# Kernel optimization log

Hardware: AMD Instinct MI355X
Metric: run time of the kernel (lower is better)

## Reference

```python
import jax, jax.numpy as jnp
import numpy as np

EPS = 1e-5  # InstanceNorm2d default eps


def setup_inputs() -> dict:
    key = jax.random.key(0)
    ks = jax.random.split(key, 5)
    B, T, C, N, H = 4, 8, 256, 196, 4
    s = 1.0 / np.sqrt(C)
    return {
        "emb": jax.random.normal(ks[0], (B, T, C, N), dtype=jnp.float32),
        "Wq": jax.random.normal(ks[1], (H, C, C), dtype=jnp.float32) * s,
        "Wk": jax.random.normal(ks[2], (H, C, C), dtype=jnp.float32) * s,
        "Wv": jax.random.normal(ks[3], (H, C, C), dtype=jnp.float32) * s,
        "Wo": jax.random.normal(ks[4], (C, C), dtype=jnp.float32) * s,
    }


def reference(emb, Wq, Wk, Wv, Wo):
    B, T, C, N = emb.shape
    S = T * N  # KV_size
    # emb.permute(0,1,3,2).view(B, T*N, C)
    x = jnp.transpose(emb, (0, 1, 3, 2)).reshape(B, S, C)
    # per-head full-width Linear projections (nn.Linear: y = x @ W.T)
    Q = jnp.einsum("bsc,hdc->bhsd", x, Wq)  # [B,H,S,C]
    K = jnp.einsum("bsc,hdc->bhsd", x, Wk)
    V = jnp.einsum("bsc,hdc->bhsd", x, Wv)
    scores = jnp.einsum("bhsd,bhtd->bhst", Q, K) / jnp.sqrt(jnp.float32(S))
    # InstanceNorm2d over each [S,S] map per (batch, head), no affine, biased var
    mean = jnp.mean(scores, axis=(-2, -1), keepdims=True)
    var = jnp.var(scores, axis=(-2, -1), keepdims=True)
    normed = (scores - mean) * jax.lax.rsqrt(var + EPS)
    probs = jax.nn.softmax(normed, axis=-1)  # attn_dropout: eval-mode identity
    ctx = jnp.einsum("bhst,bhtd->bhsd", probs, V)  # [B,H,S,C]
    ctx = jnp.mean(ctx, axis=1)  # mean over heads -> [B,S,C]
    O1 = jnp.einsum("bsc,dc->bsd", ctx, Wo)  # out Linear; proj_dropout identity
    # .view(-1, num_frames, num_channels, num_patches) on contiguous [B, T*N, C]
    return O1.reshape(B, T, C, N)
```

## Files before the change

kernel.cpp:

```cpp
#include <hip/hip_runtime.h>
#include <stdint.h>

typedef unsigned short u16;

#define Bb 4
#define Hh 4
#define Tt 8
#define Cc 256
#define NP 196
#define Ss 1568
#define SCALE_S 0.0252538136f

typedef __attribute__((ext_vector_type(4))) float floatx4;
typedef __attribute__((ext_vector_type(8))) short shortx8;

__device__ __forceinline__ float bf2f(u16 u) {
    union { unsigned u; float f; } v; v.u = ((unsigned)u) << 16; return v.f;
}
__device__ __forceinline__ u16 f2bf(float f) {
    union { float f; unsigned u; } v; v.f = f;
    unsigned r = v.u + 0x7FFFu + ((v.u >> 16) & 1u);
    return (u16)(r >> 16);
}

__global__ __launch_bounds__(256) void k_convw(const float* __restrict__ src, u16* __restrict__ dst, int n) {
    int i = blockIdx.x * 256 + threadIdx.x;
    if (i < n) dst[i] = f2bf(src[i]);
}

__device__ __forceinline__ void mfma_step(const u16* As, const u16* Bs, int lane,
                                          int wm, int wn, floatx4 acc[4][4]) {
    const int r15 = lane & 15;
    const int kq  = (lane >> 4) << 3;
    shortx8 a[4], b[4];
#pragma unroll
    for (int i = 0; i < 4; ++i)
        a[i] = *(const shortx8*)(As + (wm * 64 + i * 16 + r15) * 32 + kq);
#pragma unroll
    for (int j = 0; j < 4; ++j)
        b[j] = *(const shortx8*)(Bs + (wn * 64 + j * 16 + r15) * 32 + kq);
#pragma unroll
    for (int i = 0; i < 4; ++i)
#pragma unroll
        for (int j = 0; j < 4; ++j)
            acc[i][j] = __builtin_amdgcn_mfma_f32_16x16x32_bf16(a[i], b[j], acc[i][j], 0, 0, 0);
}

__device__ __forceinline__ void gemm_bt_core(const u16* A, const u16* Bm, int lda, int ldb,
                                             int mbase, int mlast, int nbase, int nlast,
                                             int KD, u16* As, u16* Bs, floatx4 acc[4][4]) {
    int tid = threadIdx.x;
    int lane = tid & 63, wave = tid >> 6, wm = wave >> 1, wn = wave & 1;
    int row0 = tid >> 2, row1 = 64 + (tid >> 2);
    int cole = (tid & 3) << 3;
    for (int k0 = 0; k0 < KD; k0 += 32) {
        int ga0 = mbase + row0; ga0 = ga0 <= mlast ? ga0 : mlast;
        int ga1 = mbase + row1; ga1 = ga1 <= mlast ? ga1 : mlast;
        int gb0 = nbase + row0; gb0 = gb0 <= nlast ? gb0 : nlast;
        int gb1 = nbase + row1; gb1 = gb1 <= nlast ? gb1 : nlast;
        shortx8 va0 = *(const shortx8*)(A  + (size_t)ga0 * lda + k0 + cole);
        shortx8 va1 = *(const shortx8*)(A  + (size_t)ga1 * lda + k0 + cole);
        shortx8 vb0 = *(const shortx8*)(Bm + (size_t)gb0 * ldb + k0 + cole);
        shortx8 vb1 = *(const shortx8*)(Bm + (size_t)gb1 * ldb + k0 + cole);
        __syncthreads();
        *(shortx8*)(As + row0 * 32 + cole) = va0;
        *(shortx8*)(As + row1 * 32 + cole) = va1;
        *(shortx8*)(Bs + row0 * 32 + cole) = vb0;
        *(shortx8*)(Bs + row1 * 32 + cole) = vb1;
        __syncthreads();
        mfma_step(As, Bs, lane, wm, wn, acc);
    }
}

__global__ void k_transpose(const float* __restrict__ emb, u16* __restrict__ x) {
    __shared__ u16 tile[32][33];
    int bt = blockIdx.z;
    int c0 = blockIdx.y * 32, n0 = blockIdx.x * 32;
    const float* src = emb + (size_t)bt * Cc * NP;
#pragma unroll
    for (int rr = 0; rr < 32; rr += 8) {
        int c = c0 + threadIdx.y + rr;
        int n = n0 + threadIdx.x;
        u16 v = 0;
        if (n < NP) v = f2bf(src[(size_t)c * NP + n]);
        tile[threadIdx.y + rr][threadIdx.x] = v;
    }
    __syncthreads();
    int b = bt / Tt, t = bt % Tt;
    u16* dst = x + ((size_t)b * Ss + (size_t)t * NP) * Cc;
#pragma unroll
    for (int rr = 0; rr < 32; rr += 8) {
        int n = n0 + threadIdx.y + rr;
        int c = c0 + threadIdx.x;
        if (n < NP) dst[(size_t)n * Cc + c] = tile[threadIdx.x][threadIdx.y + rr];
    }
}

__global__ __launch_bounds__(256) void k_qkv(const u16* __restrict__ x,
                                             const u16* __restrict__ Wq,
                                             const u16* __restrict__ Wk,
                                             const u16* __restrict__ Wv,
                                             u16* __restrict__ Q, u16* __restrict__ Kb,
                                             u16* __restrict__ Vt) {
    __shared__ __align__(16) u16 As[128 * 32], Bs[128 * 32];
    floatx4 acc[4][4];
#pragma unroll
    for (int i = 0; i < 4; ++i)
#pragma unroll
        for (int j = 0; j < 4; ++j) acc[i][j] = (floatx4)(0.f);
    int z = blockIdx.z;
    int qkv = z >> 4, bh = z & 15, b = bh >> 2, h = bh & 3;
    const u16* A = x + (size_t)b * Ss * Cc;
    const u16* W = (qkv == 0 ? Wq : (qkv == 1 ? Wk : Wv)) + (size_t)h * Cc * Cc;
    int mbase = blockIdx.y * 128, nbase = blockIdx.x * 128;
    gemm_bt_core(A, W, Cc, Cc, mbase, Ss - 1, nbase, Cc - 1, Cc, As, Bs, acc);

    int tid = threadIdx.x, lane = tid & 63, wave = tid >> 6, wm = wave >> 1, wn = wave & 1;
    int rq = (lane >> 4) << 2, cn = lane & 15;
    if (qkv < 2) {
        u16* out = (qkv == 0 ? Q : Kb) + (size_t)bh * Ss * Cc;
#pragma unroll
        for (int i = 0; i < 4; ++i) {
            int mb = mbase + wm * 64 + i * 16 + rq;
#pragma unroll
            for (int j = 0; j < 4; ++j) {
                int n = nbase + wn * 64 + j * 16 + cn;
#pragma unroll
                for (int r = 0; r < 4; ++r) {
                    int m = mb + r;
                    if (m < Ss) out[(size_t)m * Cc + n] = f2bf(acc[i][j][r]);
                }
            }
        }
    } else {
        u16* out = Vt + (size_t)bh * Cc * Ss;
#pragma unroll
        for (int i = 0; i < 4; ++i) {
            int m0 = mbase + wm * 64 + i * 16 + rq;
            if (m0 < Ss) {
#pragma unroll
                for (int j = 0; j < 4; ++j) {
                    int n = nbase + wn * 64 + j * 16 + cn;
                    ushort4 v;
                    v.x = f2bf(acc[i][j][0]); v.y = f2bf(acc[i][j][1]);
                    v.z = f2bf(acc[i][j][2]); v.w = f2bf(acc[i][j][3]);
                    *(ushort4*)(out + (size_t)n * Ss + m0) = v;
                }
            }
        }
    }
}

__global__ __launch_bounds__(256) void k_scores(const u16* __restrict__ Q,
                                                const u16* __restrict__ Kb,
                                                u16* __restrict__ Sc, float* __restrict__ stats) {
    __shared__ __align__(16) u16 As[128 * 32], Bs[128 * 32];
    __shared__ float sred[8];
    floatx4 acc[4][4];
#pragma unroll
    for (int i = 0; i < 4; ++i)
#pragma unroll
        for (int j = 0; j < 4; ++j) acc[i][j] = (floatx4)(0.f);
    int bh = blockIdx.z;
    const u16* A  = Q  + (size_t)bh * Ss * Cc;
    const u16* Bm = Kb + (size_t)bh * Ss * Cc;
    int mbase = blockIdx.y * 128, nbase = blockIdx.x * 128;
    gemm_bt_core(A, Bm, Cc, Cc, mbase, Ss - 1, nbase, Ss - 1, Cc, As, Bs, acc);

    int tid = threadIdx.x, lane = tid & 63, wave = tid >> 6, wm = wave >> 1, wn = wave & 1;
    int rq = (lane >> 4) << 2, cn = lane & 15;
    u16* out = Sc + (size_t)bh * Ss * Ss;
    float lsum = 0.f, lsq = 0.f;
#pragma unroll
    for (int i = 0; i < 4; ++i) {
        int mb = mbase + wm * 64 + i * 16 + rq;
#pragma unroll
        for (int j = 0; j < 4; ++j) {
            int n = nbase + wn * 64 + j * 16 + cn;
            bool nv = n < Ss;
#pragma unroll
            for (int r = 0; r < 4; ++r) {
                int m = mb + r;
                if (nv && m < Ss) {
                    float v = acc[i][j][r] * SCALE_S;
                    out[(size_t)m * Ss + n] = f2bf(v);
                    lsum += v; lsq += v * v;
                }
            }
        }
    }
#pragma unroll
    for (int mk = 1; mk <= 32; mk <<= 1) { lsum += __shfl_xor(lsum, mk); lsq += __shfl_xor(lsq, mk); }
    if (lane == 0) { sred[wave] = lsum; sred[4 + wave] = lsq; }
    __syncthreads();
    if (tid == 0) atomicAdd(&stats[bh * 4 + 0], sred[0] + sred[1] + sred[2] + sred[3]);
    if (tid == 1) atomicAdd(&stats[bh * 4 + 1], sred[4] + sred[5] + sred[6] + sred[7]);
}

__global__ void k_stats(float* __restrict__ stats) {
    int i = threadIdx.x;
    if (i < 16) {
        float inv  = 1.f / ((float)Ss * (float)Ss);
        float mean = stats[i * 4] * inv;
        float var  = stats[i * 4 + 1] * inv - mean * mean;
        var = fmaxf(var, 0.f);
        stats[i * 4 + 2] = mean;
        stats[i * 4 + 3] = rsqrtf(var + 1e-5f);
    }
}

__global__ __launch_bounds__(256) void k_pv(const u16* __restrict__ Sc,
                                            const u16* __restrict__ Vt,
                                            const float* __restrict__ stats,
                                            u16* __restrict__ ctx) {
    __shared__ __align__(16) u16 As[128 * 32], Bs[128 * 32];
    __shared__ float rs[128];
    floatx4 acc[4][4];
#pragma unroll
    for (int i = 0; i < 4; ++i)
#pragma unroll
        for (int j = 0; j < 4; ++j) acc[i][j] = (floatx4)(0.f);
    int bh = blockIdx.z;
    float mean = stats[bh * 4 + 2], istd = stats[bh * 4 + 3];
    float aa = istd * 1.44269504f;
    float bb = -mean * aa;
    const u16* A  = Sc + (size_t)bh * Ss * Ss;
    const u16* Bm = Vt + (size_t)bh * Cc * Ss;
    int mbase = blockIdx.y * 128, nbase = blockIdx.x * 128;
    int tid = threadIdx.x, lane = tid & 63, wave = tid >> 6, wm = wave >> 1, wn = wave & 1;
    int row0 = tid >> 2, row1 = 64 + (tid >> 2);
    int cole = (tid & 3) << 3;
    float rsum0 = 0.f, rsum1 = 0.f;

    for (int k0 = 0; k0 < Ss; k0 += 32) {
        int ga0 = mbase + row0; ga0 = ga0 <= Ss - 1 ? ga0 : Ss - 1;
        int ga1 = mbase + row1; ga1 = ga1 <= Ss - 1 ? ga1 : Ss - 1;
        shortx8 v0 = *(const shortx8*)(A + (size_t)ga0 * Ss + k0 + cole);
        shortx8 v1 = *(const shortx8*)(A + (size_t)ga1 * Ss + k0 + cole);
        shortx8 vb0 = *(const shortx8*)(Bm + (size_t)(nbase + row0) * Ss + k0 + cole);
        shortx8 vb1 = *(const shortx8*)(Bm + (size_t)(nbase + row1) * Ss + k0 + cole);
        shortx8 o0, o1;
        float p0 = 0.f, p1 = 0.f;
#pragma unroll
        for (int e = 0; e < 8; ++e) {
            float f0 = bf2f((u16)v0[e]);
            float e0 = exp2f(f0 * aa + bb);
            p0 += e0; o0[e] = (short)f2bf(e0);
            float f1 = bf2f((u16)v1[e]);
            float e1 = exp2f(f1 * aa + bb);
            p1 += e1; o1[e] = (short)f2bf(e1);
        }
        rsum0 += p0; rsum1 += p1;
        __syncthreads();
        *(shortx8*)(As + row0 * 32 + cole) = o0;
        *(shortx8*)(As + row1 * 32 + cole) = o1;
        *(shortx8*)(Bs + row0 * 32 + cole) = vb0;
        *(shortx8*)(Bs + row1 * 32 + cole) = vb1;
        __syncthreads();
        mfma_step(As, Bs, lane, wm, wn, acc);
    }
    rsum0 += __shfl_xor(rsum0, 1); rsum0 += __shfl_xor(rsum0, 2);
    rsum1 += __shfl_xor(rsum1, 1); rsum1 += __shfl_xor(rsum1, 2);
    __syncthreads();
    if ((tid & 3) == 0) { rs[tid >> 2] = rsum0; rs[64 + (tid >> 2)] = rsum1; }
    __syncthreads();

    u16* out = ctx + (size_t)bh * Ss * Cc;
    int rq = (lane >> 4) << 2, cn = lane & 15;
#pragma unroll
    for (int i = 0; i < 4; ++i) {
        int ml = wm * 64 + i * 16 + rq;
#pragma unroll
        for (int r = 0; r < 4; ++r) {
            int m = mbase + ml + r;
            if (m < Ss) {
                float invs = 1.f / rs[ml + r];
#pragma unroll
                for (int j = 0; j < 4; ++j) {
                    int n = nbase + wn * 64 + j * 16 + cn;
                    out[(size_t)m * Cc + n] = f2bf(acc[i][j][r] * invs);
                }
            }
        }
    }
}

__global__ __launch_bounds__(256) void k_hmean(const u16* __restrict__ ctx, u16* __restrict__ ctxm) {
    int i = blockIdx.x * 256 + threadIdx.x;
    const int PB = Ss * Cc / 4;
    int b = i / PB, g = i % PB;
    float a0 = 0.f, a1 = 0.f, a2 = 0.f, a3 = 0.f;
#pragma unroll
    for (int h = 0; h < Hh; ++h) {
        ushort4 v = *((const ushort4*)(ctx + ((size_t)(b * Hh + h)) * Ss * Cc) + g);
        a0 += bf2f(v.x); a1 += bf2f(v.y); a2 += bf2f(v.z); a3 += bf2f(v.w);
    }
    ushort4 o;
    o.x = f2bf(a0 * 0.25f); o.y = f2bf(a1 * 0.25f);
    o.z = f2bf(a2 * 0.25f); o.w = f2bf(a3 * 0.25f);
    *((ushort4*)(ctxm + (size_t)b * Ss * Cc) + g) = o;
}

__global__ __launch_bounds__(256) void k_out(const u16* __restrict__ ctxm,
                                             const u16* __restrict__ Wo, float* __restrict__ out) {
    __shared__ __align__(16) u16 As[128 * 32], Bs[128 * 32];
    floatx4 acc[4][4];
#pragma unroll
    for (int i = 0; i < 4; ++i)
#pragma unroll
        for (int j = 0; j < 4; ++j) acc[i][j] = (floatx4)(0.f);
    int b = blockIdx.z;
    const u16* A = ctxm + (size_t)b * Ss * Cc;
    int mbase = blockIdx.y * 128, nbase = blockIdx.x * 128;
    gemm_bt_core(A, Wo, Cc, Cc, mbase, Ss - 1, nbase, Cc - 1, Cc, As, Bs, acc);

    int tid = threadIdx.x, lane = tid & 63, wave = tid >> 6, wm = wave >> 1, wn = wave & 1;
    int rq = (lane >> 4) << 2, cn = lane & 15;
    float* o = out + (size_t)b * Ss * Cc;
#pragma unroll
    for (int i = 0; i < 4; ++i) {
        int mb = mbase + wm * 64 + i * 16 + rq;
#pragma unroll
        for (int j = 0; j < 4; ++j) {
            int n = nbase + wn * 64 + j * 16 + cn;
#pragma unroll
            for (int r = 0; r < 4; ++r) {
                int m = mb + r;
                if (m < Ss) o[(size_t)m * Cc + n] = acc[i][j][r];
            }
        }
    }
}

extern "C" void kernel_launch(void* const* d_in, const int* in_sizes, int n_in,
                              void* d_out, int out_size, void* d_ws, size_t ws_size,
                              hipStream_t stream) {
    const float* emb = (const float*)d_in[0];
    float* out = (float*)d_out;

    char* ws = (char*)d_ws;
    size_t off = 0;
    auto alloc = [&](size_t bytes) -> void* {
        void* p = ws + off;
        off = (off + bytes + 255) & ~(size_t)255;
        return p;
    };
    float* stats = (float*)alloc(16 * 4 * sizeof(float));
    u16* Wqc  = (u16*)alloc((size_t)Hh * Cc * Cc * 2);
    u16* Wkc  = (u16*)alloc((size_t)Hh * Cc * Cc * 2);
    u16* Wvc  = (u16*)alloc((size_t)Hh * Cc * Cc * 2);
    u16* Woc  = (u16*)alloc((size_t)Cc * Cc * 2);
    u16* x    = (u16*)alloc((size_t)Bb * Ss * Cc * 2);
    u16* Q    = (u16*)alloc((size_t)Bb * Hh * Ss * Cc * 2);
    u16* Kb   = (u16*)alloc((size_t)Bb * Hh * Ss * Cc * 2);
    u16* Vt   = (u16*)alloc((size_t)Bb * Hh * Ss * Cc * 2);
    u16* ctxm = (u16*)alloc((size_t)Bb * Ss * Cc * 2);
    u16* Sc   = (u16*)alloc((size_t)Bb * Hh * Ss * Ss * 2);
    u16* ctx  = Q;

    hipMemsetAsync(stats, 0, 16 * 4 * sizeof(float), stream);

    k_convw<<<dim3(1024), dim3(256), 0, stream>>>((const float*)d_in[1], Wqc, Hh * Cc * Cc);
    k_convw<<<dim3(1024), dim3(256), 0, stream>>>((const float*)d_in[2], Wkc, Hh * Cc * Cc);
    k_convw<<<dim3(1024), dim3(256), 0, stream>>>((const float*)d_in[3], Wvc, Hh * Cc * Cc);
    k_convw<<<dim3(256),  dim3(256), 0, stream>>>((const float*)d_in[4], Woc, Cc * Cc);

    k_transpose<<<dim3(7, 8, 32), dim3(32, 8), 0, stream>>>(emb, x);
    k_qkv<<<dim3(2, 13, 48), dim3(256), 0, stream>>>(x, Wqc, Wkc, Wvc, Q, Kb, Vt);
    k_scores<<<dim3(13, 13, 16), dim3(256), 0, stream>>>(Q, Kb, Sc, stats);
    k_stats<<<dim3(1), dim3(64), 0, stream>>>(stats);
    k_pv<<<dim3(2, 13, 16), dim3(256), 0, stream>>>(Sc, Vt, stats, ctx);
    k_hmean<<<dim3(1568), dim3(256), 0, stream>>>(ctx, ctxm);
    k_out<<<dim3(2, 13, 4), dim3(256), 0, stream>>>(ctxm, Woc, out);
}
```

Before: 262.3 us.

## Fuse head-mean into PV via atomics and register-prefetch next K tile in GEMMs

Removes the k_hmean kernel. k_pv now atomically adds its 0.25-scaled, row-normalised output straight into an fp32 ctxm buffer that is zeroed with a memset. k_out reads ctxm as fp32 and converts it to bf16 while staging. The shared GEMM core, k_pv and k_out also prefetch the next k-slice into registers before the MFMA step, so global loads overlap compute. The aim is to drop one kernel launch and the bf16 per-head ctx round trip, at the cost of fp32 atomic contention, a larger fp32 buffer and an extra memset.

Result: faster. 255.1 us (-2.7%).

```diff
diff --git a/kernel.cpp b/kernel.cpp
--- a/kernel.cpp
+++ b/kernel.cpp
@@ -53,20 +53,31 @@
     int lane = tid & 63, wave = tid >> 6, wm = wave >> 1, wn = wave & 1;
     int row0 = tid >> 2, row1 = 64 + (tid >> 2);
     int cole = (tid & 3) << 3;
+    int ga0 = mbase + row0; ga0 = ga0 <= mlast ? ga0 : mlast;
+    int ga1 = mbase + row1; ga1 = ga1 <= mlast ? ga1 : mlast;
+    int gb0 = nbase + row0; gb0 = gb0 <= nlast ? gb0 : nlast;
+    int gb1 = nbase + row1; gb1 = gb1 <= nlast ? gb1 : nlast;
+    const u16* pa0 = A  + (size_t)ga0 * lda + cole;
+    const u16* pa1 = A  + (size_t)ga1 * lda + cole;
+    const u16* pb0 = Bm + (size_t)gb0 * ldb + cole;
+    const u16* pb1 = Bm + (size_t)gb1 * ldb + cole;
+    shortx8 va0 = *(const shortx8*)(pa0);
+    shortx8 va1 = *(const shortx8*)(pa1);
+    shortx8 vb0 = *(const shortx8*)(pb0);
+    shortx8 vb1 = *(const shortx8*)(pb1);
     for (int k0 = 0; k0 < KD; k0 += 32) {
-        int ga0 = mbase + row0; ga0 = ga0 <= mlast ? ga0 : mlast;
-        int ga1 = mbase + row1; ga1 = ga1 <= mlast ? ga1 : mlast;
-        int gb0 = nbase + row0; gb0 = gb0 <= nlast ? gb0 : nlast;
-        int gb1 = nbase + row1; gb1 = gb1 <= nlast ? gb1 : nlast;
-        shortx8 va0 = *(const shortx8*)(A  + (size_t)ga0 * lda + k0 + cole);
-        shortx8 va1 = *(const shortx8*)(A  + (size_t)ga1 * lda + k0 + cole);
-        shortx8 vb0 = *(const shortx8*)(Bm + (size_t)gb0 * ldb + k0 + cole);
-        shortx8 vb1 = *(const shortx8*)(Bm + (size_t)gb1 * ldb + k0 + cole);
         __syncthreads();
         *(shortx8*)(As + row0 * 32 + cole) = va0;
         *(shortx8*)(As + row1 * 32 + cole) = va1;
         *(shortx8*)(Bs + row0 * 32 + cole) = vb0;
         *(shortx8*)(Bs + row1 * 32 + cole) = vb1;
+        int k1 = k0 + 32;
+        if (k1 < KD) {
+            va0 = *(const shortx8*)(pa0 + k1);
+            va1 = *(const shortx8*)(pa1 + k1);
+            vb0 = *(const shortx8*)(pb0 + k1);
+            vb1 = *(const shortx8*)(pb1 + k1);
+        }
         __syncthreads();
         mfma_step(As, Bs, lane, wm, wn, acc);
     }
@@ -212,7 +223,7 @@
 __global__ __launch_bounds__(256) void k_pv(const u16* __restrict__ Sc,
                                             const u16* __restrict__ Vt,
                                             const float* __restrict__ stats,
-                                            u16* __restrict__ ctx) {
+                                            float* __restrict__ ctxm) {
     __shared__ __align__(16) u16 As[128 * 32], Bs[128 * 32];
     __shared__ float rs[128];
     floatx4 acc[4][4];
@@ -230,15 +241,19 @@
     int tid = threadIdx.x, lane = tid & 63, wave = tid >> 6, wm = wave >> 1, wn = wave & 1;
     int row0 = tid >> 2, row1 = 64 + (tid >> 2);
     int cole = (tid & 3) << 3;
+    int ga0 = mbase + row0; ga0 = ga0 <= Ss - 1 ? ga0 : Ss - 1;
+    int ga1 = mbase + row1; ga1 = ga1 <= Ss - 1 ? ga1 : Ss - 1;
+    const u16* pa0 = A + (size_t)ga0 * Ss + cole;
+    const u16* pa1 = A + (size_t)ga1 * Ss + cole;
+    const u16* pb0 = Bm + (size_t)(nbase + row0) * Ss + cole;
+    const u16* pb1 = Bm + (size_t)(nbase + row1) * Ss + cole;
     float rsum0 = 0.f, rsum1 = 0.f;
+    shortx8 v0 = *(const shortx8*)(pa0);
+    shortx8 v1 = *(const shortx8*)(pa1);
+    shortx8 vb0 = *(const shortx8*)(pb0);
+    shortx8 vb1 = *(const shortx8*)(pb1);
 
     for (int k0 = 0; k0 < Ss; k0 += 32) {
-        int ga0 = mbase + row0; ga0 = ga0 <= Ss - 1 ? ga0 : Ss - 1;
-        int ga1 = mbase + row1; ga1 = ga1 <= Ss - 1 ? ga1 : Ss - 1;
-        shortx8 v0 = *(const shortx8*)(A + (size_t)ga0 * Ss + k0 + cole);
-        shortx8 v1 = *(const shortx8*)(A + (size_t)ga1 * Ss + k0 + cole);
-        shortx8 vb0 = *(const shortx8*)(Bm + (size_t)(nbase + row0) * Ss + k0 + cole);
-        shortx8 vb1 = *(const shortx8*)(Bm + (size_t)(nbase + row1) * Ss + k0 + cole);
         shortx8 o0, o1;
         float p0 = 0.f, p1 = 0.f;
 #pragma unroll
@@ -256,6 +271,13 @@
         *(shortx8*)(As + row1 * 32 + cole) = o1;
         *(shortx8*)(Bs + row0 * 32 + cole) = vb0;
         *(shortx8*)(Bs + row1 * 32 + cole) = vb1;
+        int k1 = k0 + 32;
+        if (k1 < Ss) {
+            v0  = *(const shortx8*)(pa0 + k1);
+            v1  = *(const shortx8*)(pa1 + k1);
+            vb0 = *(const shortx8*)(pb0 + k1);
+            vb1 = *(const shortx8*)(pb1 + k1);
+        }
         __syncthreads();
         mfma_step(As, Bs, lane, wm, wn, acc);
     }
@@ -265,7 +287,8 @@
     if ((tid & 3) == 0) { rs[tid >> 2] = rsum0; rs[64 + (tid >> 2)] = rsum1; }
     __syncthreads();
 
-    u16* out = ctx + (size_t)bh * Ss * Cc;
+    int b = bh >> 2;
+    float* outp = ctxm + (size_t)b * Ss * Cc;
     int rq = (lane >> 4) << 2, cn = lane & 15;
 #pragma unroll
     for (int i = 0; i < 4; ++i) {
@@ -274,34 +297,18 @@
         for (int r = 0; r < 4; ++r) {
             int m = mbase + ml + r;
             if (m < Ss) {
-                float invs = 1.f / rs[ml + r];
+                float invs = 0.25f / rs[ml + r];
 #pragma unroll
                 for (int j = 0; j < 4; ++j) {
                     int n = nbase + wn * 64 + j * 16 + cn;
-                    out[(size_t)m * Cc + n] = f2bf(acc[i][j][r] * invs);
+                    atomicAdd(&outp[(size_t)m * Cc + n], acc[i][j][r] * invs);
                 }
             }
         }
     }
 }
 
-__global__ __launch_bounds__(256) void k_hmean(const u16* __restrict__ ctx, u16* __restrict__ ctxm) {
-    int i = blockIdx.x * 256 + threadIdx.x;
-    const int PB = Ss * Cc / 4;
-    int b = i / PB, g = i % PB;
-    float a0 = 0.f, a1 = 0.f, a2 = 0.f, a3 = 0.f;
-#pragma unroll
-    for (int h = 0; h < Hh; ++h) {
-        ushort4 v = *((const ushort4*)(ctx + ((size_t)(b * Hh + h)) * Ss * Cc) + g);
-        a0 += bf2f(v.x); a1 += bf2f(v.y); a2 += bf2f(v.z); a3 += bf2f(v.w);
-    }
-    ushort4 o;
-    o.x = f2bf(a0 * 0.25f); o.y = f2bf(a1 * 0.25f);
-    o.z = f2bf(a2 * 0.25f); o.w = f2bf(a3 * 0.25f);
-    *((ushort4*)(ctxm + (size_t)b * Ss * Cc) + g) = o;
-}
-
-__global__ __launch_bounds__(256) void k_out(const u16* __restrict__ ctxm,
+__global__ __launch_bounds__(256) void k_out(const float* __restrict__ ctxm,
                                              const u16* __restrict__ Wo, float* __restrict__ out) {
     __shared__ __align__(16) u16 As[128 * 32], Bs[128 * 32];
     floatx4 acc[4][4];
@@ -310,11 +317,42 @@
 #pragma unroll
         for (int j = 0; j < 4; ++j) acc[i][j] = (floatx4)(0.f);
     int b = blockIdx.z;
-    const u16* A = ctxm + (size_t)b * Ss * Cc;
+    const float* A = ctxm + (size_t)b * Ss * Cc;
     int mbase = blockIdx.y * 128, nbase = blockIdx.x * 128;
-    gemm_bt_core(A, Wo, Cc, Cc, mbase, Ss - 1, nbase, Cc - 1, Cc, As, Bs, acc);
-
     int tid = threadIdx.x, lane = tid & 63, wave = tid >> 6, wm = wave >> 1, wn = wave & 1;
+    int row0 = tid >> 2, row1 = 64 + (tid >> 2);
+    int cole = (tid & 3) << 3;
+    int ga0 = mbase + row0; ga0 = ga0 <= Ss - 1 ? ga0 : Ss - 1;
+    int ga1 = mbase + row1; ga1 = ga1 <= Ss - 1 ? ga1 : Ss - 1;
+    const float* pa0 = A + (size_t)ga0 * Cc + cole;
+    const float* pa1 = A + (size_t)ga1 * Cc + cole;
+    const u16* pb0 = Wo + (size_t)(nbase + row0 <= Cc - 1 ? nbase + row0 : Cc - 1) * Cc + cole;
+    const u16* pb1 = Wo + (size_t)(nbase + row1 <= Cc - 1 ? nbase + row1 : Cc - 1) * Cc + cole;
+    float4 a00 = *(const float4*)(pa0), a01 = *(const float4*)(pa0 + 4);
+    float4 a10 = *(const float4*)(pa1), a11 = *(const float4*)(pa1 + 4);
+    shortx8 vb0 = *(const shortx8*)(pb0);
+    shortx8 vb1 = *(const shortx8*)(pb1);
+    for (int k0 = 0; k0 < Cc; k0 += 32) {
+        shortx8 o0, o1;
+        o0[0] = (short)f2bf(a00.x); o0[1] = (short)f2bf(a00.y); o0[2] = (short)f2bf(a00.z); o0[3] = (short)f2bf(a00.w);
+        o0[4] = (short)f2bf(a01.x); o0[5] = (short)f2bf(a01.y); o0[6] = (short)f2bf(a01.z); o0[7] = (short)f2bf(a01.w);
+        o1[0] = (short)f2bf(a10.x); o1[1] = (short)f2bf(a10.y); o1[2] = (short)f2bf(a10.z); o1[3] = (short)f2bf(a10.w);
+        o1[4] = (short)f2bf(a11.x); o1[5] = (short)f2bf(a11.y); o1[6] = (short)f2bf(a11.z); o1[7] = (short)f2bf(a11.w);
+        __syncthreads();
+        *(shortx8*)(As + row0 * 32 + cole) = o0;
+        *(shortx8*)(As + row1 * 32 + cole) = o1;
+        *(shortx8*)(Bs + row0 * 32 + cole) = vb0;
+        *(shortx8*)(Bs + row1 * 32 + cole) = vb1;
+        int k1 = k0 + 32;
+        if (k1 < Cc) {
+            a00 = *(const float4*)(pa0 + k1); a01 = *(const float4*)(pa0 + k1 + 4);
+            a10 = *(const float4*)(pa1 + k1); a11 = *(const float4*)(pa1 + k1 + 4);
+            vb0 = *(const shortx8*)(pb0 + k1);
+            vb1 = *(const shortx8*)(pb1 + k1);
+        }
+        __syncthreads();
+        mfma_step(As, Bs, lane, wm, wn, acc);
+    }
     int rq = (lane >> 4) << 2, cn = lane & 15;
     float* o = out + (size_t)b * Ss * Cc;
 #pragma unroll
@@ -354,11 +392,11 @@
     u16* Q    = (u16*)alloc((size_t)Bb * Hh * Ss * Cc * 2);
     u16* Kb   = (u16*)alloc((size_t)Bb * Hh * Ss * Cc * 2);
     u16* Vt   = (u16*)alloc((size_t)Bb * Hh * Ss * Cc * 2);
-    u16* ctxm = (u16*)alloc((size_t)Bb * Ss * Cc * 2);
+    float* ctxm = (float*)alloc((size_t)Bb * Ss * Cc * 4);
     u16* Sc   = (u16*)alloc((size_t)Bb * Hh * Ss * Ss * 2);
-    u16* ctx  = Q;
 
     hipMemsetAsync(stats, 0, 16 * 4 * sizeof(float), stream);
+    hipMemsetAsync(ctxm, 0, (size_t)Bb * Ss * Cc * 4, stream);
 
     k_convw<<<dim3(1024), dim3(256), 0, stream>>>((const float*)d_in[1], Wqc, Hh * Cc * Cc);
     k_convw<<<dim3(1024), dim3(256), 0, stream>>>((const float*)d_in[2], Wkc, Hh * Cc * Cc);
@@ -369,7 +407,6 @@
     k_qkv<<<dim3(2, 13, 48), dim3(256), 0, stream>>>(x, Wqc, Wkc, Wvc, Q, Kb, Vt);
     k_scores<<<dim3(13, 13, 16), dim3(256), 0, stream>>>(Q, Kb, Sc, stats);
     k_stats<<<dim3(1), dim3(64), 0, stream>>>(stats);
-    k_pv<<<dim3(2, 13, 16), dim3(256), 0, stream>>>(Sc, Vt, stats, ctx);
-    k_hmean<<<dim3(1568), dim3(256), 0, stream>>>(ctx, ctxm);
+    k_pv<<<dim3(2, 13, 16), dim3(256), 0, stream>>>(Sc, Vt, stats, ctxm);
     k_out<<<dim3(2, 13, 4), dim3(256), 0, stream>>>(ctxm, Woc, out);
 }
```
